# Optimization experiments

Measured on AMD Instinct MI355X. Metric: run time of the kernel, lower is better.

The kernel has to match this reference:

```python
import jax, jax.numpy as jnp
import numpy as np

H = 1024   # x-axis resolution
W = 1024   # y-axis resolution
HID = 256  # hidden_size (image setting per paper)
C = 3      # RGB out_channels


def _siren_uniform(key, shape, fan_in):
    b = np.sqrt(6.0 / fan_in)
    return jax.random.uniform(key, shape, minval=-b, maxval=b, dtype=jnp.float32)


def setup_inputs() -> dict:
    key = jax.random.key(0)
    ks = jax.random.split(key, 16)
    x = jax.random.uniform(ks[0], (H, 1), minval=-1.0, maxval=1.0, dtype=jnp.float32)
    y = jax.random.uniform(ks[1], (W, 1), minval=-1.0, maxval=1.0, dtype=jnp.float32)
    return {
        "x": x, "y": y,
        # per-axis branch Linear(1, HID)
        "bw0": _siren_uniform(ks[2], (HID, 1), 1), "bb0": _siren_uniform(ks[3], (HID,), 1),
        "bw1": _siren_uniform(ks[4], (HID, 1), 1), "bb1": _siren_uniform(ks[5], (HID,), 1),
        # shared premerge: Sine -> Linear -> Sine -> Linear -> Sine
        "pw1": _siren_uniform(ks[6], (HID, HID), HID), "pb1": _siren_uniform(ks[7], (HID,), HID),
        "pw2": _siren_uniform(ks[8], (HID, HID), HID), "pb2": _siren_uniform(ks[9], (HID,), HID),
        # postmerge: Linear -> Sine -> Linear -> Sigmoid
        "qw1": _siren_uniform(ks[10], (HID, HID), HID), "qb1": _siren_uniform(ks[11], (HID,), HID),
        "qw2": _siren_uniform(ks[12], (C, HID), HID), "qb2": _siren_uniform(ks[13], (C,), HID),
    }


def reference(x, y, bw0, bb0, bw1, bb1, pw1, pb1, pw2, pb2, qw1, qb1, qw2, qb2):
    def premerge(h):
        # Sine(w0=1) -> Linear -> Sine -> Linear -> Sine
        h = jnp.sin(h)
        h = jnp.sin(h @ pw1.T + pb1)
        h = jnp.sin(h @ pw2.T + pb2)
        return h

    fx = premerge(x @ bw0.T + bb0)  # [H, HID]
    fy = premerge(y @ bw1.T + bb1)  # [W, HID]
    merged = jnp.einsum('ik,jk->ijk', fx, fy)          # [H, W, HID] outer-product fusion
    h = jnp.sin(merged @ qw1.T + qb1)                  # [H, W, HID]
    out = jax.nn.sigmoid(h @ qw2.T + qb2)              # [H, W, C]
    return jnp.transpose(out, (2, 1, 0))               # [C, W, H]
```

## Files before the change

kernel.cpp:

```cpp
#include <hip/hip_runtime.h>

#define HH  1024
#define WW  1024
#define HID 256

typedef __attribute__((ext_vector_type(4))) float f32x4;
typedef __attribute__((ext_vector_type(8))) short short8;

static __device__ __forceinline__ unsigned short f2bf(float x) {
    unsigned u = __builtin_bit_cast(unsigned, x);
    u = (u + 0x7fffu + ((u >> 16) & 1u)) >> 16;
    return (unsigned short)u;
}


__global__ __launch_bounds__(256) void transpose_k(
    const float* __restrict__ pw1, const float* __restrict__ pw2,
    float* __restrict__ pw1t, float* __restrict__ pw2t)
{
    __shared__ float tile[32][33];
    const float* src = blockIdx.z ? pw2 : pw1;
    float*       dst = blockIdx.z ? pw2t : pw1t;
    const int bx = blockIdx.x * 32, by = blockIdx.y * 32;
    const int tx = threadIdx.x & 31, ty0 = threadIdx.x >> 5;
    #pragma unroll
    for (int r = 0; r < 32; r += 8)
        tile[ty0 + r][tx] = src[(by + ty0 + r) * HID + bx + tx];
    __syncthreads();
    #pragma unroll
    for (int r = 0; r < 32; r += 8)
        dst[(bx + ty0 + r) * HID + by + tx] = tile[tx][ty0 + r];
}

__global__ __launch_bounds__(256) void branch_k(
    const float* __restrict__ x, const float* __restrict__ y,
    const float* __restrict__ bw0, const float* __restrict__ bb0,
    const float* __restrict__ bw1, const float* __restrict__ bb1,
    float* __restrict__ s0)
{
    const int t  = threadIdx.x;
    const int g0 = blockIdx.x * 8;
    const int axis = g0 >> 10;
    const float* coord = axis ? y : x;
    const float* bw = axis ? bw1 : bw0;
    const float* bb = axis ? bb1 : bb0;
    const int base = g0 & 1023;
    const float wv = bw[t], bv = bb[t];
    #pragma unroll
    for (int q = 0; q < 8; ++q)
        s0[(g0 + q) * HID + t] = __sinf(coord[base + q] * wv + bv);
}

__global__ __launch_bounds__(256) void layer_k(
    const float* __restrict__ sin_in,
    const float* __restrict__ wt,
    const float* __restrict__ bias,
    float* __restrict__ sout,
    unsigned short* __restrict__ fx_b, float* __restrict__ fy_f,
    const int is_final)
{
    const int t  = threadIdx.x;
    const int g0 = blockIdx.x * 8;
    float acc[8];
    const float bv = bias[t];
    #pragma unroll
    for (int q = 0; q < 8; ++q) acc[q] = bv;
    const float* srow = sin_in + g0 * HID;
    for (int c = 0; c < HID; ++c) {
        const float wv = wt[c * HID + t];
        #pragma unroll
        for (int q = 0; q < 8; ++q) acc[q] += srow[q * HID + c] * wv;
    }
    if (!is_final) {
        #pragma unroll
        for (int q = 0; q < 8; ++q) sout[(g0 + q) * HID + t] = __sinf(acc[q]);
    } else {
        #pragma unroll
        for (int q = 0; q < 8; ++q) {
            const float h = __sinf(acc[q]);
            const int g = g0 + q;
            if (g < HH) fx_b[g * HID + t] = f2bf(h);
            else        fy_f[(g - HH) * HID + t] = h;
        }
    }
}

__global__ __launch_bounds__(256, 3) void fused_k(
    const float* __restrict__ qw1, const float* __restrict__ qb1,
    const float* __restrict__ qw2,
    const unsigned short* __restrict__ fx_b, const float* __restrict__ fy_f,
    float* __restrict__ pout)
{
    const int j    = blockIdx.x >> 1;
    const int half = blockIdx.x & 1;
    const int tid  = threadIdx.x;
    const int l    = tid & 63;
    const int w    = tid >> 6;
    const int n0   = half * 128 + w * 32;
    const int il   = l & 15;
    const int lg   = l >> 4;

    float qb1r[2][4], qw2r[3][2][4];
    #pragma unroll
    for (int nt = 0; nt < 2; ++nt) {
        #pragma unroll
        for (int r = 0; r < 4; ++r) {
            const int n = n0 + nt * 16 + lg * 4 + r;
            qb1r[nt][r]    = qb1[n];
            qw2r[0][nt][r] = qw2[0 * HID + n];
            qw2r[1][nt][r] = qw2[1 * HID + n];
            qw2r[2][nt][r] = qw2[2 * HID + n];
        }
    }

    short8 afrag[2][8];
    #pragma unroll
    for (int kt = 0; kt < 8; ++kt) {
        const int kb = kt * 32 + lg * 8;
        const f32x4 fA = *(const f32x4*)&fy_f[j * HID + kb];
        const f32x4 fB = *(const f32x4*)&fy_f[j * HID + kb + 4];
        #pragma unroll
        for (int nt = 0; nt < 2; ++nt) {
            const int n = n0 + nt * 16 + il;
            const f32x4 qA = *(const f32x4*)&qw1[n * HID + kb];
            const f32x4 qB = *(const f32x4*)&qw1[n * HID + kb + 4];
            short8 f;
            f[0] = (short)f2bf(qA[0] * fA[0]);
            f[1] = (short)f2bf(qA[1] * fA[1]);
            f[2] = (short)f2bf(qA[2] * fA[2]);
            f[3] = (short)f2bf(qA[3] * fA[3]);
            f[4] = (short)f2bf(qB[0] * fB[0]);
            f[5] = (short)f2bf(qB[1] * fB[1]);
            f[6] = (short)f2bf(qB[2] * fB[2]);
            f[7] = (short)f2bf(qB[3] * fB[3]);
            afrag[nt][kt] = f;
        }
    }

    __shared__ __attribute__((aligned(16))) char tile[2][8192];
    __shared__ float red[4][3][256];

    unsigned swz[2];
    #pragma unroll
    for (int r = 0; r < 2; ++r) {
        const unsigned f = w * 2 + r;
        swz[r] = (unsigned)(il * 512 + lg * 16 + (f & 3) * 64 + (f >> 2) * 256);
    }
    const char* fxb = (const char*)fx_b;

    #pragma unroll
    for (int r = 0; r < 2; ++r)
        __builtin_amdgcn_global_load_lds(
            (const __attribute__((address_space(1))) unsigned*)(fxb + swz[r]),
            (__attribute__((address_space(3))) unsigned*)(&tile[0][(w * 2 + r) * 1024 + l * 16]),
            16, 0, 0);
    __syncthreads();

    int itg = 0;
    for (int seg = 0; seg < 4; ++seg) {
        for (int it16 = 0; it16 < 16; ++it16, ++itg) {
            const int buf = itg & 1;
            if (itg < 63) {
                const char* src = fxb + (unsigned)(itg + 1) * 8192u;
                #pragma unroll
                for (int r = 0; r < 2; ++r)
                    __builtin_amdgcn_global_load_lds(
                        (const __attribute__((address_space(1))) unsigned*)(src + swz[r]),
                        (__attribute__((address_space(3))) unsigned*)(&tile[buf ^ 1][(w * 2 + r) * 1024 + l * 16]),
                        16, 0, 0);
            }
            f32x4 acc[2];
            #pragma unroll
            for (int nt = 0; nt < 2; ++nt) {
                acc[nt][0] = qb1r[nt][0]; acc[nt][1] = qb1r[nt][1];
                acc[nt][2] = qb1r[nt][2]; acc[nt][3] = qb1r[nt][3];
            }
            const char* tb = &tile[buf][l * 16];
            #pragma unroll
            for (int g = 0; g < 2; ++g) {
                short8 bfrag[4];
                #pragma unroll
                for (int kk = 0; kk < 4; ++kk)
                    bfrag[kk] = *(const short8*)(tb + (g * 4 + kk) * 1024);
                #pragma unroll
                for (int kk = 0; kk < 4; ++kk) {
                    #pragma unroll
                    for (int nt = 0; nt < 2; ++nt)
                        acc[nt] = __builtin_amdgcn_mfma_f32_16x16x32_bf16(
                            afrag[nt][g * 4 + kk], bfrag[kk], acc[nt], 0, 0, 0);
                }
            }
            float p0 = 0.f, p1 = 0.f, p2 = 0.f;
            #pragma unroll
            for (int nt = 0; nt < 2; ++nt) {
                #pragma unroll
                for (int r = 0; r < 4; ++r) {
                    const float s = __sinf(acc[nt][r]);
                    p0 += qw2r[0][nt][r] * s;
                    p1 += qw2r[1][nt][r] * s;
                    p2 += qw2r[2][nt][r] * s;
                }
            }
            p0 += __shfl_xor(p0, 16); p0 += __shfl_xor(p0, 32);
            p1 += __shfl_xor(p1, 16); p1 += __shfl_xor(p1, 32);
            p2 += __shfl_xor(p2, 16); p2 += __shfl_xor(p2, 32);
            if (l < 16) {
                const int ic = it16 * 16 + l;
                red[w][0][ic] = p0;
                red[w][1][ic] = p1;
                red[w][2][ic] = p2;
            }
            __syncthreads();
        }
        {
            const int ib = j * HH + seg * 256 + tid;
            #pragma unroll
            for (int q = 0; q < 3; ++q) {
                const float v = red[0][q][tid] + red[1][q][tid]
                              + red[2][q][tid] + red[3][q][tid];
                pout[(half * 3 + q) * (WW * HH) + ib] = v;
            }
        }
        __syncthreads();
    }
}

__global__ __launch_bounds__(256) void combine_k(
    const float* __restrict__ part, const float* __restrict__ qb2,
    float* __restrict__ out)
{
    const int t = blockIdx.x * 256 + threadIdx.x;
    const int c = t >> 18;
    const f32x4 a = ((const f32x4*)part)[t];
    const f32x4 b = ((const f32x4*)(part + 3 * WW * HH))[t];
    const float bias = qb2[c];
    f32x4 o;
    #pragma unroll
    for (int q = 0; q < 4; ++q)
        o[q] = 1.0f / (1.0f + __expf(-(a[q] + b[q] + bias)));
    ((f32x4*)out)[t] = o;
}

extern "C" void kernel_launch(void* const* d_in, const int* in_sizes, int n_in,
                              void* d_out, int out_size, void* d_ws, size_t ws_size,
                              hipStream_t stream)
{
    const float* x   = (const float*)d_in[0];
    const float* y   = (const float*)d_in[1];
    const float* bw0 = (const float*)d_in[2];
    const float* bb0 = (const float*)d_in[3];
    const float* bw1 = (const float*)d_in[4];
    const float* bb1 = (const float*)d_in[5];
    const float* pw1 = (const float*)d_in[6];
    const float* pb1 = (const float*)d_in[7];
    const float* pw2 = (const float*)d_in[8];
    const float* pb2 = (const float*)d_in[9];
    const float* qw1 = (const float*)d_in[10];
    const float* qb1 = (const float*)d_in[11];
    const float* qw2 = (const float*)d_in[12];
    const float* qb2 = (const float*)d_in[13];

    char* ws = (char*)d_ws;
    unsigned short* fx_b = (unsigned short*)(ws);
    float* fy_f = (float*)(ws + (512 << 10));
    float* pw1t = (float*)(ws + (1536 << 10));
    float* pw2t = (float*)(ws + (1792 << 10));
    float* s0   = (float*)(ws + (2048 << 10));
    float* s1   = (float*)(ws + (4096 << 10));
    float* part = (float*)(ws + (8192 << 10));
    float* out  = (float*)d_out;

    transpose_k<<<dim3(8, 8, 2), 256, 0, stream>>>(pw1, pw2, pw1t, pw2t);
    branch_k<<<256, 256, 0, stream>>>(x, y, bw0, bb0, bw1, bb1, s0);
    layer_k<<<256, 256, 0, stream>>>(s0, pw1t, pb1, s1, nullptr, nullptr, 0);
    layer_k<<<256, 256, 0, stream>>>(s1, pw2t, pb2, nullptr, fx_b, fy_f, 1);
    fused_k<<<2 * WW, 256, 0, stream>>>(qw1, qb1, qw2, fx_b, fy_f, part);
    combine_k<<<(3 * WW * HH / 4) / 256, 256, 0, stream>>>(part, qb2, out);
}
```

Baseline: 278.7 us.

## Triple-buffer fx tiles with partial vmcnt waits to deepen prefetch

Turns the double-buffered LDS tile pipeline into a triple-buffered one that keeps two tile loads in flight. Each per-iteration __syncthreads becomes a barrier preceded by s_waitcnt vmcnt(2), so the current tile's loads are drained while the next loads stay outstanding. The goal is to hide more global-to-LDS latency behind the MFMA work. The cost is an extra 8KB of LDS per block, which may lower occupancy, plus two redundant wrap-around loads at the end. The hand-written waitcnt also depends on the exact number of outstanding vector memory ops, which the compiler may not preserve.

```diff
diff --git a/kernel.cpp b/kernel.cpp
--- a/kernel.cpp
+++ b/kernel.cpp
@@ -137,7 +137,7 @@
         }
     }
 
-    __shared__ __attribute__((aligned(16))) char tile[2][8192];
+    __shared__ __attribute__((aligned(16))) char tile[3][8192];
     __shared__ float red[4][3][256];
 
     unsigned swz[2];
@@ -148,26 +148,35 @@
     }
     const char* fxb = (const char*)fx_b;
 
-    #pragma unroll
-    for (int r = 0; r < 2; ++r)
-        __builtin_amdgcn_global_load_lds(
-            (const __attribute__((address_space(1))) unsigned*)(fxb + swz[r]),
-            (__attribute__((address_space(3))) unsigned*)(&tile[0][(w * 2 + r) * 1024 + l * 16]),
-            16, 0, 0);
-    __syncthreads();
+#define STAGE(slot, tidx)                                                        \
+    do {                                                                         \
+        const char* _src = fxb + (unsigned)(tidx) * 8192u;                       \
+        _Pragma("unroll")                                                        \
+        for (int _r = 0; _r < 2; ++_r)                                           \
+            __builtin_amdgcn_global_load_lds(                                    \
+                (const __attribute__((address_space(1))) unsigned*)(_src + swz[_r]), \
+                (__attribute__((address_space(3))) unsigned*)(&tile[slot][(w * 2 + _r) * 1024 + l * 16]), \
+                16, 0, 0);                                                       \
+    } while (0)
+
+#define WAITBAR asm volatile("s_waitcnt vmcnt(2)\n\ts_barrier" ::: "memory")
+
+    STAGE(0, 0);
+    STAGE(1, 1);
+    WAITBAR;
 
     int itg = 0;
+    int cur = 0;
     for (int seg = 0; seg < 4; ++seg) {
         for (int it16 = 0; it16 < 16; ++it16, ++itg) {
-            const int buf = itg & 1;
-            if (itg < 63) {
-                const char* src = fxb + (unsigned)(itg + 1) * 8192u;
-                #pragma unroll
-                for (int r = 0; r < 2; ++r)
-                    __builtin_amdgcn_global_load_lds(
-                        (const __attribute__((address_space(1))) unsigned*)(src + swz[r]),
-                        (__attribute__((address_space(3))) unsigned*)(&tile[buf ^ 1][(w * 2 + r) * 1024 + l * 16]),
-                        16, 0, 0);
+            {
+                int s2 = cur + 2; if (s2 >= 3) s2 -= 3;
+                const int tidx = (itg + 2) & 63;
+                switch (s2) {
+                    case 0: STAGE(0, tidx); break;
+                    case 1: STAGE(1, tidx); break;
+                    default: STAGE(2, tidx); break;
+                }
             }
             f32x4 acc[2];
             #pragma unroll
@@ -175,7 +184,7 @@
                 acc[nt][0] = qb1r[nt][0]; acc[nt][1] = qb1r[nt][1];
                 acc[nt][2] = qb1r[nt][2]; acc[nt][3] = qb1r[nt][3];
             }
-            const char* tb = &tile[buf][l * 16];
+            const char* tb = &tile[cur][l * 16];
             #pragma unroll
             for (int g = 0; g < 2; ++g) {
                 short8 bfrag[4];
@@ -210,7 +219,8 @@
                 red[w][1][ic] = p1;
                 red[w][2][ic] = p2;
             }
-            __syncthreads();
+            WAITBAR;
+            cur = cur + 1 == 3 ? 0 : cur + 1;
         }
         {
             const int ib = j * HH + seg * 256 + tid;
@@ -221,8 +231,10 @@
                 pout[(half * 3 + q) * (WW * HH) + ib] = v;
             }
         }
-        __syncthreads();
-    }
+        asm volatile("s_barrier" ::: "memory");
+    }
+#undef STAGE
+#undef WAITBAR
 }
 
 __global__ __launch_bounds__(256) void combine_k(
```

Measured after the change: 250.9 us. 10.0% less time.

## Pre-swizzle fx into MFMA fragment layout and load B fragments directly from global

Applied to the files above, without the earlier changes.

The final premerge layer now writes the bf16 fx tensor in a tiled layout that matches the MFMA B-fragment order. This lets fused_k read each fragment with direct 16-byte global loads instead of staging it through a double-buffered LDS tile with global_load_lds. With no LDS tile, the per-iteration __syncthreads is replaced by one barrier per segment, and the occupancy hint is dropped from launch_bounds. The cost is that fragment loads now hit L2/global with no explicit prefetch, and all four waves load the same data independently.

```diff
diff --git a/kernel.cpp b/kernel.cpp
--- a/kernel.cpp
+++ b/kernel.cpp
@@ -56,7 +56,7 @@
     const float* __restrict__ wt,
     const float* __restrict__ bias,
     float* __restrict__ sout,
-    unsigned short* __restrict__ fx_b, float* __restrict__ fy_f,
+    unsigned short* __restrict__ fxT, float* __restrict__ fy_f,
     const int is_final)
 {
     const int t  = threadIdx.x;
@@ -75,20 +75,26 @@
         #pragma unroll
         for (int q = 0; q < 8; ++q) sout[(g0 + q) * HID + t] = __sinf(acc[q]);
     } else {
+        const int f  = ((t >> 7) << 2) | ((t >> 5) & 3);
+        const int lg = (t >> 3) & 3, e = t & 7;
         #pragma unroll
         for (int q = 0; q < 8; ++q) {
             const float h = __sinf(acc[q]);
             const int g = g0 + q;
-            if (g < HH) fx_b[g * HID + t] = f2bf(h);
-            else        fy_f[(g - HH) * HID + t] = h;
-        }
-    }
-}
-
-__global__ __launch_bounds__(256, 3) void fused_k(
+            if (g < HH) {
+                const int ti = g >> 4, il = g & 15;
+                fxT[ti * 4096 + f * 512 + (lg * 16 + il) * 8 + e] = f2bf(h);
+            } else {
+                fy_f[(g - HH) * HID + t] = h;
+            }
+        }
+    }
+}
+
+__global__ __launch_bounds__(256) void fused_k(
     const float* __restrict__ qw1, const float* __restrict__ qb1,
     const float* __restrict__ qw2,
-    const unsigned short* __restrict__ fx_b, const float* __restrict__ fy_f,
+    const unsigned short* __restrict__ fxT, const float* __restrict__ fy_f,
     float* __restrict__ pout)
 {
     const int j    = blockIdx.x >> 1;
@@ -137,58 +143,31 @@
         }
     }
 
-    __shared__ __attribute__((aligned(16))) char tile[2][8192];
     __shared__ float red[4][3][256];
 
-    unsigned swz[2];
-    #pragma unroll
-    for (int r = 0; r < 2; ++r) {
-        const unsigned f = w * 2 + r;
-        swz[r] = (unsigned)(il * 512 + lg * 16 + (f & 3) * 64 + (f >> 2) * 256);
-    }
-    const char* fxb = (const char*)fx_b;
-
-    #pragma unroll
-    for (int r = 0; r < 2; ++r)
-        __builtin_amdgcn_global_load_lds(
-            (const __attribute__((address_space(1))) unsigned*)(fxb + swz[r]),
-            (__attribute__((address_space(3))) unsigned*)(&tile[0][(w * 2 + r) * 1024 + l * 16]),
-            16, 0, 0);
-    __syncthreads();
-
-    int itg = 0;
+    const unsigned short* fxl = fxT + l * 8;
+
     for (int seg = 0; seg < 4; ++seg) {
-        for (int it16 = 0; it16 < 16; ++it16, ++itg) {
-            const int buf = itg & 1;
-            if (itg < 63) {
-                const char* src = fxb + (unsigned)(itg + 1) * 8192u;
-                #pragma unroll
-                for (int r = 0; r < 2; ++r)
-                    __builtin_amdgcn_global_load_lds(
-                        (const __attribute__((address_space(1))) unsigned*)(src + swz[r]),
-                        (__attribute__((address_space(3))) unsigned*)(&tile[buf ^ 1][(w * 2 + r) * 1024 + l * 16]),
-                        16, 0, 0);
-            }
+        #pragma unroll 2
+        for (int it16 = 0; it16 < 16; ++it16) {
+            const int itg = seg * 16 + it16;
+            const unsigned short* tb = fxl + itg * 4096;
+            short8 bfrag[8];
+            #pragma unroll
+            for (int f = 0; f < 8; ++f)
+                bfrag[f] = *(const short8*)(tb + f * 512);
             f32x4 acc[2];
             #pragma unroll
             for (int nt = 0; nt < 2; ++nt) {
                 acc[nt][0] = qb1r[nt][0]; acc[nt][1] = qb1r[nt][1];
                 acc[nt][2] = qb1r[nt][2]; acc[nt][3] = qb1r[nt][3];
             }
-            const char* tb = &tile[buf][l * 16];
-            #pragma unroll
-            for (int g = 0; g < 2; ++g) {
-                short8 bfrag[4];
+            #pragma unroll
+            for (int f = 0; f < 8; ++f) {
                 #pragma unroll
-                for (int kk = 0; kk < 4; ++kk)
-                    bfrag[kk] = *(const short8*)(tb + (g * 4 + kk) * 1024);
-                #pragma unroll
-                for (int kk = 0; kk < 4; ++kk) {
-                    #pragma unroll
-                    for (int nt = 0; nt < 2; ++nt)
-                        acc[nt] = __builtin_amdgcn_mfma_f32_16x16x32_bf16(
-                            afrag[nt][g * 4 + kk], bfrag[kk], acc[nt], 0, 0, 0);
-                }
+                for (int nt = 0; nt < 2; ++nt)
+                    acc[nt] = __builtin_amdgcn_mfma_f32_16x16x32_bf16(
+                        afrag[nt][f], bfrag[f], acc[nt], 0, 0, 0);
             }
             float p0 = 0.f, p1 = 0.f, p2 = 0.f;
             #pragma unroll
@@ -210,8 +189,8 @@
                 red[w][1][ic] = p1;
                 red[w][2][ic] = p2;
             }
-            __syncthreads();
-        }
+        }
+        __syncthreads();
         {
             const int ib = j * HH + seg * 256 + tid;
             #pragma unroll
@@ -261,7 +240,7 @@
     const float* qb2 = (const float*)d_in[13];
 
     char* ws = (char*)d_ws;
-    unsigned short* fx_b = (unsigned short*)(ws);
+    unsigned short* fxT = (unsigned short*)(ws);
     float* fy_f = (float*)(ws + (512 << 10));
     float* pw1t = (float*)(ws + (1536 << 10));
     float* pw2t = (float*)(ws + (1792 << 10));
@@ -273,7 +252,7 @@
     transpose_k<<<dim3(8, 8, 2), 256, 0, stream>>>(pw1, pw2, pw1t, pw2t);
     branch_k<<<256, 256, 0, stream>>>(x, y, bw0, bb0, bw1, bb1, s0);
     layer_k<<<256, 256, 0, stream>>>(s0, pw1t, pb1, s1, nullptr, nullptr, 0);
-    layer_k<<<256, 256, 0, stream>>>(s1, pw2t, pb2, nullptr, fx_b, fy_f, 1);
-    fused_k<<<2 * WW, 256, 0, stream>>>(qw1, qb1, qw2, fx_b, fy_f, part);
+    layer_k<<<256, 256, 0, stream>>>(s1, pw2t, pb2, nullptr, fxT, fy_f, 1);
+    fused_k<<<2 * WW, 256, 0, stream>>>(qw1, qb1, qw2, fxT, fy_f, part);
     combine_k<<<(3 * WW * HH / 4) / 256, 256, 0, stream>>>(part, qb2, out);
 }
```

New measurement: 318.8 us. +14.4%, slower.
